# Optimization experiments

Hardware: AMD Instinct MI355X
Metric: run time of the kernel (lower is better)

## Reference

```python
import jax, jax.numpy as jnp
import numpy as np

TEMPERATURE = 0.7
BIG_NEG = -1e30  # safe stand-in for -inf (keeps grads finite)


def setup_inputs() -> dict:
    key = jax.random.key(0)
    k1, k2, k3 = jax.random.split(key, 3)
    B, D = 8192, 256
    embeddings = jax.random.normal(k1, (B, D), dtype=jnp.float32)
    categories = jax.random.randint(k2, (B,), 0, 16, dtype=jnp.int64)
    font_labels = jax.random.randint(k3, (B,), 0, 2000, dtype=jnp.int64)
    return {"embeddings": embeddings, "categories": categories, "font_labels": font_labels}


def reference(embeddings, categories, font_labels):
    # L2-normalize rows
    e = embeddings / jnp.linalg.norm(embeddings, axis=1, keepdims=True)
    sims = jnp.matmul(e, e.T) / TEMPERATURE  # [B, B]
    B = sims.shape[0]

    same = categories[:, None] == categories[None, :]
    diag = jnp.eye(B, dtype=bool)
    pos_mask = same & ~diag           # same category, excluding self
    neg_mask = ~same                  # different category (self excluded implicitly)

    valid = pos_mask.any(axis=1) & neg_mask.any(axis=1)

    pos_sim = jnp.max(jnp.where(pos_mask, sims, BIG_NEG), axis=1)  # hardest positive per anchor
    neg_max = jnp.max(jnp.where(neg_mask, sims, BIG_NEG), axis=1)

    # logsumexp over {pos_sim} U neg_sims, numerically stable
    m = jnp.where(valid, jnp.maximum(pos_sim, neg_max), 0.0)
    pos_safe = jnp.where(valid, pos_sim, 0.0)
    exp_neg_sum = jnp.sum(jnp.where(neg_mask, jnp.exp(sims - m[:, None]), 0.0), axis=1)
    lse = m + jnp.log(jnp.exp(pos_safe - m) + exp_neg_sum)

    loss_per_anchor = -pos_safe + lse
    n_valid = jnp.maximum(jnp.sum(valid), 1)
    return jnp.sum(jnp.where(valid, loss_per_anchor, 0.0)) / n_valid
```

## Files before the change

### kernel.cpp

```cpp
#include <hip/hip_runtime.h>
#include <stdint.h>

#define NROWS 8192
#define DDIM 256
#define NSTRIPS 16
#define STRIP_COLS 512
#define BN 32
#define NTILES 16
#define BM 128

#define ESCALE 1.4356159f
#define LN2F   0.6931471806f
#define NEGBIG (-1e30f)

typedef __attribute__((ext_vector_type(8))) short short8;
typedef __attribute__((ext_vector_type(4))) float f32x4;

typedef __attribute__((address_space(3))) void lds_void;
typedef const __attribute__((address_space(1))) void gl_void;

__device__ __forceinline__ unsigned short f2bf(float x) {
  unsigned int u = __float_as_uint(x);
  u += 0x7fffu + ((u >> 16) & 1u);
  return (unsigned short)(u >> 16);
}

__global__ __launch_bounds__(256) void knorm(const float* __restrict__ emb,
                                             unsigned short* __restrict__ ebf) {
  const int wave = threadIdx.x >> 6, lane = threadIdx.x & 63;
  const int row = blockIdx.x * 4 + wave;
  const float4 v = *(const float4*)(emb + row * DDIM + lane * 4);
  float ss = v.x * v.x + v.y * v.y + v.z * v.z + v.w * v.w;
#pragma unroll
  for (int off = 1; off < 64; off <<= 1) ss += __shfl_xor(ss, off, 64);
  const float sc = rsqrtf(ss) * ESCALE;
  ushort4 o;
  o.x = f2bf(v.x * sc); o.y = f2bf(v.y * sc);
  o.z = f2bf(v.z * sc); o.w = f2bf(v.w * sc);
  *(ushort4*)(ebf + row * DDIM + lane * 4) = o;
}

__global__ __launch_bounds__(256) void kmain(const unsigned short* __restrict__ ebf,
                                             const int* __restrict__ cats,
                                             float* __restrict__ posP,
                                             float* __restrict__ sumP) {
  __shared__ alignas(16) unsigned short smem[2][BN * DDIM];
  const int tid = threadIdx.x;
  const int lane = tid & 63, wave = tid >> 6;
  const int lane15 = lane & 15, quad = lane >> 4;
  const int strip = blockIdx.x, rowTile = blockIdx.y;
  const int rowG = rowTile * BM + wave * 32;
  const int col0 = strip * STRIP_COLS;

  short8 a[2][8];
#pragma unroll
  for (int m = 0; m < 2; ++m)
#pragma unroll
    for (int kk = 0; kk < 8; ++kk)
      a[m][kk] = *(const short8*)(ebf + (rowG + m * 16 + lane15) * DDIM + kk * 32 + quad * 8);

  int cati[2][4];
#pragma unroll
  for (int m = 0; m < 2; ++m)
#pragma unroll
    for (int r = 0; r < 4; ++r)
      cati[m][r] = cats[rowG + m * 16 + quad * 4 + r];

  bool dlr[4];
#pragma unroll
  for (int r = 0; r < 4; ++r) dlr[r] = (lane15 == quad * 4 + r);

  float pm[2][4], ns[2][4];
#pragma unroll
  for (int m = 0; m < 2; ++m)
#pragma unroll
    for (int r = 0; r < 4; ++r) { pm[m][r] = NEGBIG; ns[m][r] = 0.f; }

#define STAGE(t, buf)                                                           \
  {                                                                             \
    const unsigned short* g = ebf +                                             \
        (size_t)(col0 + (t) * BN + (lane & 31)) * DDIM +                        \
        (wave * 2 + (lane >> 5)) * 8;                                           \
    char* lb = (char*)&smem[(buf)][0] + wave * 1024;                            \
    _Pragma("unroll")                                                           \
    for (int c = 0; c < 4; ++c)                                                 \
      __builtin_amdgcn_global_load_lds((gl_void*)(g + c * 64),                  \
                                       (lds_void*)(lb + c * 4096), 16, 0, 0);   \
  }

  STAGE(0, 0);

  for (int t = 0; t < NTILES; ++t) {
    __syncthreads();
    if (t + 1 < NTILES) STAGE(t + 1, (t + 1) & 1);
    const char* bb = (const char*)&smem[t & 1][0];
    const int colBase = col0 + t * BN;
    const int cjt[2] = {cats[colBase + lane15], cats[colBase + 16 + lane15]};

#pragma unroll
    for (int nt = 0; nt < 2; ++nt) {
      f32x4 acc0 = {0.f, 0.f, 0.f, 0.f}, acc1 = {0.f, 0.f, 0.f, 0.f};
#pragma unroll
      for (int kk = 0; kk < 8; ++kk) {
        short8 b = *(const short8*)(bb + kk * 2048 + quad * 512 + nt * 256 + lane15 * 16);
        acc0 = __builtin_amdgcn_mfma_f32_16x16x32_bf16(a[0][kk], b, acc0, 0, 0, 0);
        acc1 = __builtin_amdgcn_mfma_f32_16x16x32_bf16(a[1][kk], b, acc1, 0, 0, 0);
      }
      const int cj = cjt[nt];
      const bool dg0 = (rowG == colBase + nt * 16);
      const bool dg1 = (rowG + 16 == colBase + nt * 16);
#pragma unroll
      for (int m = 0; m < 2; ++m) {
        const bool dg = m ? dg1 : dg0;
#pragma unroll
        for (int r = 0; r < 4; ++r) {
          const float s = m ? acc1[r] : acc0[r];
          const float e = __builtin_amdgcn_exp2f(s);
          const bool same = (cj == cati[m][r]);
          float psv = same ? s : NEGBIG;
          if (dg) psv = dlr[r] ? NEGBIG : psv;
          pm[m][r] = fmaxf(pm[m][r], psv);
          ns[m][r] += same ? 0.f : e;
        }
      }
    }
  }

#pragma unroll
  for (int off = 1; off < 16; off <<= 1) {
#pragma unroll
    for (int m = 0; m < 2; ++m)
#pragma unroll
      for (int r = 0; r < 4; ++r) {
        pm[m][r] = fmaxf(pm[m][r], __shfl_xor(pm[m][r], off, 64));
        ns[m][r] += __shfl_xor(ns[m][r], off, 64);
      }
  }
  if (lane15 == 0) {
#pragma unroll
    for (int m = 0; m < 2; ++m)
#pragma unroll
      for (int r = 0; r < 4; ++r) {
        const int row = rowG + m * 16 + quad * 4 + r;
        posP[strip * NROWS + row] = pm[m][r];
        sumP[strip * NROWS + row] = ns[m][r];
      }
  }
}

__global__ __launch_bounds__(256) void kmerge(const float* __restrict__ posP,
                                              const float* __restrict__ sumP,
                                              float* __restrict__ acc,
                                              float* __restrict__ out) {
  const int row = blockIdx.x * 256 + threadIdx.x;
  float pm = NEGBIG, ns = 0.f;
#pragma unroll
  for (int s = 0; s < NSTRIPS; ++s) {
    pm = fmaxf(pm, posP[s * NROWS + row]);
    ns += sumP[s * NROWS + row];
  }
  const bool valid = (pm > -1e29f) && (ns > 0.f);
  float loss = valid ? (logf(__builtin_amdgcn_exp2f(pm) + ns) - pm * LN2F) : 0.f;
  float cnt = valid ? 1.f : 0.f;
#pragma unroll
  for (int off = 1; off < 64; off <<= 1) {
    loss += __shfl_xor(loss, off, 64);
    cnt += __shfl_xor(cnt, off, 64);
  }
  if ((threadIdx.x & 63) == 0) {
    atomicAdd(&acc[0], loss);
    atomicAdd(&acc[1], cnt);
    __threadfence();
  }
  __syncthreads();
  if (threadIdx.x == 0) {
    const int prev = atomicAdd((int*)(acc + 2), 1);
    if (prev == (int)gridDim.x - 1) {
      const float L = atomicAdd(&acc[0], 0.f);
      const float C = atomicAdd(&acc[1], 0.f);
      out[0] = L / fmaxf(C, 1.f);
    }
  }
}

extern "C" void kernel_launch(void* const* d_in, const int* in_sizes, int n_in,
                              void* d_out, int out_size, void* d_ws, size_t ws_size,
                              hipStream_t stream) {
  const float* emb = (const float*)d_in[0];
  const int* cats = (const int*)d_in[1];
  float* out = (float*)d_out;

  char* ws = (char*)d_ws;
  float* accv = (float*)ws;
  unsigned short* ebf = (unsigned short*)(ws + 256);
  float* posP = (float*)(ws + 256 + NROWS * DDIM * 2);
  float* sumP = posP + NSTRIPS * NROWS;

  hipMemsetAsync(accv, 0, 16, stream);
  knorm<<<NROWS / 4, 256, 0, stream>>>(emb, ebf);
  kmain<<<dim3(NSTRIPS, NROWS / BM), 256, 0, stream>>>(ebf, cats, posP, sumP);
  kmerge<<<NROWS / 256, 256, 0, stream>>>(posP, sumP, accv, out);
}
```

Baseline: 119.9 us.

## Fuse merge into main kernel, drop LDS staging, fold memset into norm kernel

Removes the LDS double-buffered B-tile staging and loads B fragments straight from global memory into registers, processing 16 columns per step with unroll 2 and launch bounds requesting 3 blocks per SM. The separate merge kernel is folded into kmain: the last 32 blocks to finish take a ticket, spin until all blocks are done, then reduce the per-strip partials, which removes a kernel launch. The accumulator memset moves into knorm, removing another launch. The trade-offs are that global B loads depend on L2/L1 reuse instead of shared memory, and the spin-wait in the tail blocks relies on every block being resident or already finished.

Result: slower. 248.0 us (+106.9%).

```diff
diff --git a/kernel.cpp b/kernel.cpp
--- a/kernel.cpp
+++ b/kernel.cpp
@@ -5,9 +5,10 @@
 #define DDIM 256
 #define NSTRIPS 16
 #define STRIP_COLS 512
-#define BN 32
-#define NTILES 16
 #define BM 128
+#define GRIDMAIN (NSTRIPS * (NROWS / BM))
+#define NMERGE 32
+#define MROWS (NROWS / NMERGE)
 
 #define ESCALE 1.4356159f
 #define LN2F   0.6931471806f
@@ -15,9 +16,6 @@
 
 typedef __attribute__((ext_vector_type(8))) short short8;
 typedef __attribute__((ext_vector_type(4))) float f32x4;
-
-typedef __attribute__((address_space(3))) void lds_void;
-typedef const __attribute__((address_space(1))) void gl_void;
 
 __device__ __forceinline__ unsigned short f2bf(float x) {
   unsigned int u = __float_as_uint(x);
@@ -26,7 +24,9 @@
 }
 
 __global__ __launch_bounds__(256) void knorm(const float* __restrict__ emb,
-                                             unsigned short* __restrict__ ebf) {
+                                             unsigned short* __restrict__ ebf,
+                                             float* __restrict__ accv) {
+  if (blockIdx.x == 0 && threadIdx.x < 4) accv[threadIdx.x] = 0.f;
   const int wave = threadIdx.x >> 6, lane = threadIdx.x & 63;
   const int row = blockIdx.x * 4 + wave;
   const float4 v = *(const float4*)(emb + row * DDIM + lane * 4);
@@ -40,11 +40,12 @@
   *(ushort4*)(ebf + row * DDIM + lane * 4) = o;
 }
 
-__global__ __launch_bounds__(256) void kmain(const unsigned short* __restrict__ ebf,
-                                             const int* __restrict__ cats,
-                                             float* __restrict__ posP,
-                                             float* __restrict__ sumP) {
-  __shared__ alignas(16) unsigned short smem[2][BN * DDIM];
+__global__ __launch_bounds__(256, 3) void kmain(const unsigned short* __restrict__ ebf,
+                                                const int* __restrict__ cats,
+                                                float* __restrict__ posP,
+                                                float* __restrict__ sumP,
+                                                float* __restrict__ accv,
+                                                float* __restrict__ out) {
   const int tid = threadIdx.x;
   const int lane = tid & 63, wave = tid >> 6;
   const int lane15 = lane & 15, quad = lane >> 4;
@@ -66,62 +67,52 @@
     for (int r = 0; r < 4; ++r)
       cati[m][r] = cats[rowG + m * 16 + quad * 4 + r];
 
-  bool dlr[4];
-#pragma unroll
-  for (int r = 0; r < 4; ++r) dlr[r] = (lane15 == quad * 4 + r);
-
   float pm[2][4], ns[2][4];
 #pragma unroll
   for (int m = 0; m < 2; ++m)
 #pragma unroll
     for (int r = 0; r < 4; ++r) { pm[m][r] = NEGBIG; ns[m][r] = 0.f; }
 
-#define STAGE(t, buf)                                                           \
-  {                                                                             \
-    const unsigned short* g = ebf +                                             \
-        (size_t)(col0 + (t) * BN + (lane & 31)) * DDIM +                        \
-        (wave * 2 + (lane >> 5)) * 8;                                           \
-    char* lb = (char*)&smem[(buf)][0] + wave * 1024;                            \
-    _Pragma("unroll")                                                           \
-    for (int c = 0; c < 4; ++c)                                                 \
-      __builtin_amdgcn_global_load_lds((gl_void*)(g + c * 64),                  \
-                                       (lds_void*)(lb + c * 4096), 16, 0, 0);   \
-  }
-
-  STAGE(0, 0);
-
-  for (int t = 0; t < NTILES; ++t) {
-    __syncthreads();
-    if (t + 1 < NTILES) STAGE(t + 1, (t + 1) & 1);
-    const char* bb = (const char*)&smem[t & 1][0];
-    const int colBase = col0 + t * BN;
-    const int cjt[2] = {cats[colBase + lane15], cats[colBase + 16 + lane15]};
-
-#pragma unroll
-    for (int nt = 0; nt < 2; ++nt) {
-      f32x4 acc0 = {0.f, 0.f, 0.f, 0.f}, acc1 = {0.f, 0.f, 0.f, 0.f};
-#pragma unroll
-      for (int kk = 0; kk < 8; ++kk) {
-        short8 b = *(const short8*)(bb + kk * 2048 + quad * 512 + nt * 256 + lane15 * 16);
-        acc0 = __builtin_amdgcn_mfma_f32_16x16x32_bf16(a[0][kk], b, acc0, 0, 0, 0);
-        acc1 = __builtin_amdgcn_mfma_f32_16x16x32_bf16(a[1][kk], b, acc1, 0, 0, 0);
-      }
-      const int cj = cjt[nt];
-      const bool dg0 = (rowG == colBase + nt * 16);
-      const bool dg1 = (rowG + 16 == colBase + nt * 16);
-#pragma unroll
-      for (int m = 0; m < 2; ++m) {
-        const bool dg = m ? dg1 : dg0;
-#pragma unroll
-        for (int r = 0; r < 4; ++r) {
-          const float s = m ? acc1[r] : acc0[r];
-          const float e = __builtin_amdgcn_exp2f(s);
-          const bool same = (cj == cati[m][r]);
-          float psv = same ? s : NEGBIG;
-          if (dg) psv = dlr[r] ? NEGBIG : psv;
-          pm[m][r] = fmaxf(pm[m][r], psv);
-          ns[m][r] += same ? 0.f : e;
-        }
+  const char* bp = (const char*)(ebf + (size_t)(col0 + lane15) * DDIM + quad * 8);
+  const int* cp = cats + col0 + lane15;
+
+#pragma unroll 2
+  for (int ct = 0; ct < STRIP_COLS / 16; ++ct) {
+    const int cj = cp[ct * 16];
+    short8 b[8];
+#pragma unroll
+    for (int kk = 0; kk < 8; ++kk)
+      b[kk] = *(const short8*)(bp + kk * 64);
+    bp += 16 * DDIM * 2;
+
+    f32x4 acc0 = {0.f, 0.f, 0.f, 0.f}, acc1 = {0.f, 0.f, 0.f, 0.f};
+#pragma unroll
+    for (int kk = 0; kk < 8; ++kk) {
+      acc0 = __builtin_amdgcn_mfma_f32_16x16x32_bf16(a[0][kk], b[kk], acc0, 0, 0, 0);
+      acc1 = __builtin_amdgcn_mfma_f32_16x16x32_bf16(a[1][kk], b[kk], acc1, 0, 0, 0);
+    }
+
+    const int colBase = col0 + ct * 16;
+#pragma unroll
+    for (int m = 0; m < 2; ++m) {
+      const bool dg = (rowG + m * 16 == colBase);
+      float psv[4], ev[4];
+#pragma unroll
+      for (int r = 0; r < 4; ++r) {
+        const float s = m ? acc1[r] : acc0[r];
+        const bool same = (cj == cati[m][r]);
+        psv[r] = same ? s : NEGBIG;
+        ev[r] = same ? 0.f : __builtin_amdgcn_exp2f(s);
+      }
+      if (dg) {
+#pragma unroll
+        for (int r = 0; r < 4; ++r)
+          if (lane15 == quad * 4 + r) psv[r] = NEGBIG;
+      }
+#pragma unroll
+      for (int r = 0; r < 4; ++r) {
+        pm[m][r] = fmaxf(pm[m][r], psv[r]);
+        ns[m][r] += ev[r];
       }
     }
   }
@@ -146,38 +137,49 @@
         sumP[strip * NROWS + row] = ns[m][r];
       }
   }
-}
-
-__global__ __launch_bounds__(256) void kmerge(const float* __restrict__ posP,
-                                              const float* __restrict__ sumP,
-                                              float* __restrict__ acc,
-                                              float* __restrict__ out) {
-  const int row = blockIdx.x * 256 + threadIdx.x;
-  float pm = NEGBIG, ns = 0.f;
+
+  __shared__ int sPrev;
+  __syncthreads();
+  if (tid == 0) {
+    __threadfence();
+    sPrev = atomicAdd((int*)(accv + 2), 1);
+  }
+  __syncthreads();
+  const int prev = sPrev;
+  if (prev < GRIDMAIN - NMERGE) return;
+  const int rank = prev - (GRIDMAIN - NMERGE);
+  if (tid == 0) {
+    while (atomicAdd((int*)(accv + 2), 0) < GRIDMAIN) __builtin_amdgcn_s_sleep(2);
+  }
+  __syncthreads();
+  __threadfence();
+
+  const int row = rank * MROWS + tid;
+  float pmv = NEGBIG, nsv = 0.f;
 #pragma unroll
   for (int s = 0; s < NSTRIPS; ++s) {
-    pm = fmaxf(pm, posP[s * NROWS + row]);
-    ns += sumP[s * NROWS + row];
-  }
-  const bool valid = (pm > -1e29f) && (ns > 0.f);
-  float loss = valid ? (logf(__builtin_amdgcn_exp2f(pm) + ns) - pm * LN2F) : 0.f;
+    pmv = fmaxf(pmv, atomicAdd(posP + s * NROWS + row, 0.f));
+    nsv += atomicAdd(sumP + s * NROWS + row, 0.f);
+  }
+  const bool valid = (pmv > -1e29f) && (nsv > 0.f);
+  float loss = valid ? (logf(__builtin_amdgcn_exp2f(pmv) + nsv) - pmv * LN2F) : 0.f;
   float cnt = valid ? 1.f : 0.f;
 #pragma unroll
   for (int off = 1; off < 64; off <<= 1) {
     loss += __shfl_xor(loss, off, 64);
     cnt += __shfl_xor(cnt, off, 64);
   }
-  if ((threadIdx.x & 63) == 0) {
-    atomicAdd(&acc[0], loss);
-    atomicAdd(&acc[1], cnt);
+  if (lane == 0) {
+    atomicAdd(&accv[0], loss);
+    atomicAdd(&accv[1], cnt);
+  }
+  __syncthreads();
+  if (tid == 0) {
     __threadfence();
-  }
-  __syncthreads();
-  if (threadIdx.x == 0) {
-    const int prev = atomicAdd((int*)(acc + 2), 1);
-    if (prev == (int)gridDim.x - 1) {
-      const float L = atomicAdd(&acc[0], 0.f);
-      const float C = atomicAdd(&acc[1], 0.f);
+    const int p2 = atomicAdd((int*)(accv + 3), 1);
+    if (p2 == NMERGE - 1) {
+      const float L = atomicAdd(&accv[0], 0.f);
+      const float C = atomicAdd(&accv[1], 0.f);
       out[0] = L / fmaxf(C, 1.f);
     }
   }
@@ -196,8 +198,6 @@
   float* posP = (float*)(ws + 256 + NROWS * DDIM * 2);
   float* sumP = posP + NSTRIPS * NROWS;
 
-  hipMemsetAsync(accv, 0, 16, stream);
-  knorm<<<NROWS / 4, 256, 0, stream>>>(emb, ebf);
-  kmain<<<dim3(NSTRIPS, NROWS / BM), 256, 0, stream>>>(ebf, cats, posP, sumP);
-  kmerge<<<NROWS / 256, 256, 0, stream>>>(posP, sumP, accv, out);
-}
+  knorm<<<NROWS / 4, 256, 0, stream>>>(emb, ebf, accv);
+  kmain<<<dim3(NSTRIPS, NROWS / BM), 256, 0, stream>>>(ebf, cats, posP, sumP, accv, out);
+}
```
